# Kernel optimization log

Hardware: AMD Instinct MI355X
Metric: run time of the kernel (lower is better)

The kernel has to match this reference:

```python
import jax, jax.numpy as jnp
import numpy as np

# TT config: input_dimension=2048, output_multiplier=4, rank=16
# top_ranks    = [8,2,2,2,2,2,2,2,2]  (prod = 2048)
# bottom_ranks = [8,2,2,2,2,2,2,2,2]  (prod = 2048)
# core shapes (top, bottom, left, right): left/right are TT bond ranks.
CORE_SHAPES = [(8, 8, 1, 16)] + [(2, 2, 16, 16)] * 7 + [(2, 2, 16, 1)]


def setup_inputs() -> dict:
    key = jax.random.key(0)
    ks = jax.random.split(key, 10)
    inp = {"x": jax.random.normal(ks[0], (4, 2048, 2048), dtype=jnp.float32)}
    for i, s in enumerate(CORE_SHAPES):
        inp[f"p{i}"] = jax.random.normal(ks[i + 1], s, dtype=jnp.float32)
    return inp


def _tt_apply(x, ps):
    # x: [B, S, D] with D = prod(top_ranks) = 2048
    B, S, D = x.shape
    T = B * S
    # Normalize every core to (top, bottom, left_bond_in, right_bond_out).
    # Original einsum: '... abcdefghi, ajs, bkst, cltu, dmuv, envw, fowx, gpxy, hqzy, irz -> ... jklmnopqr'
    # Core 7 ('hqzy') has swapped bonds: its 4th dim (y) is the incoming bond
    # from core 6 and its 3rd dim (z) is the outgoing bond into core 8 ('irz').
    cores = list(ps[:7]) + [jnp.transpose(ps[7], (0, 1, 3, 2)), ps[8]]
    # core 0 is used as p0[:, :, 0, :] in the original; its left dim is 1 so
    # keeping the singleton left axis is identical math.
    y = x.reshape(T, 1, 1, D)  # [T, out_so_far=1, bond=1, remaining_top=D]
    J, M = 1, D
    for g in cores:
        tk, bk, lk, rk = g.shape
        y = y.reshape(T, J, lk, tk, M // tk)
        # contract incoming bond l and current top index a with the core
        y = jnp.einsum('tjlam,ablr->tjbrm', y, g)
        J *= bk
        M //= tk
        y = y.reshape(T, J, rk, M)
    # final: rk == 1, M == 1 -> [T, J] with J = prod(bottom_ranks) = 2048
    return y.reshape(B, S, J)


def reference(x, p0, p1, p2, p3, p4, p5, p6, p7, p8):
    return _tt_apply(x, (p0, p1, p2, p3, p4, p5, p6, p7, p8))
```

## Files before the change

kernel.cpp:

```cpp
#include <hip/hip_runtime.h>
#include <stdint.h>

typedef unsigned short u16;
typedef __bf16 bf16x8 __attribute__((ext_vector_type(8)));
typedef float f32x16 __attribute__((ext_vector_type(16)));
typedef u16 u16x8 __attribute__((ext_vector_type(8)));

__device__ __forceinline__ u16 f2bf(float f) {
  uint32_t u = __float_as_uint(f);
  u += 0x7fffu + ((u >> 16) & 1u);
  return (u16)(u >> 16);
}

__global__ __launch_bounds__(256) void build_lr_kernel(
    const float* __restrict__ p0, const float* __restrict__ p1,
    const float* __restrict__ p2, const float* __restrict__ p3,
    const float* __restrict__ p4, const float* __restrict__ p5,
    const float* __restrict__ p6, const float* __restrict__ p7,
    const float* __restrict__ p8, float* __restrict__ L4, float* __restrict__ R) {
  __shared__ float sA[16384];
  __shared__ float sB[4096];
  const int tid = threadIdx.x;
  if (blockIdx.x < 16) {
    for (int i = tid; i < 1024; i += 256) sA[i] = p0[i];
    __syncthreads();
    for (int i = tid; i < 4096; i += 256) {
      int r = i & 15, t = i >> 4;
      int Bb = t & 15, Aa = t >> 4;
      int a = Aa & 1, A = Aa >> 1, b = Bb & 1, B = Bb >> 1;
      const float* srow = sA + (A * 8 + B) * 16;
      const float* g = p1 + ((a * 2 + b) * 16) * 16 + r;
      float s = 0.f;
#pragma unroll
      for (int l = 0; l < 16; l++) s += srow[l] * g[l * 16];
      sB[i] = s;
    }
    __syncthreads();
    for (int i = tid; i < 16384; i += 256) {
      int r = i & 15, t = i >> 4;
      int Bb = t & 31, Aa = t >> 5;
      int a = Aa & 1, A = Aa >> 1, b = Bb & 1, B = Bb >> 1;
      const float* srow = sB + (A * 16 + B) * 16;
      const float* g = p2 + ((a * 2 + b) * 16) * 16 + r;
      float s = 0.f;
#pragma unroll
      for (int l = 0; l < 16; l++) s += srow[l] * g[l * 16];
      sA[i] = s;
    }
    __syncthreads();
    int gi = blockIdx.x * 256 + tid;
    int b3 = gi & 1, a3 = (gi >> 1) & 1;
    int B2 = (gi >> 2) & 31, A2 = gi >> 7;
    const float* srow = sA + (A2 * 32 + B2) * 16;
    const float* g3 = p3 + ((a3 * 2 + b3) * 16) * 16;
    float tmp[16];
#pragma unroll
    for (int r3 = 0; r3 < 16; r3++) {
      float s = 0.f;
#pragma unroll
      for (int r2 = 0; r2 < 16; r2++) s += srow[r2] * g3[r2 * 16 + r3];
      tmp[r3] = s;
    }
#pragma unroll
    for (int ab = 0; ab < 4; ab++) {
      int a4 = ab >> 1, b4 = ab & 1;
      const float* g4 = p4 + (ab * 16) * 16;
      int AL = A2 * 4 + a3 * 2 + a4;
      int BL = B2 * 4 + b3 * 2 + b4;
      float* drow = L4 + (AL * 128 + BL) * 16;
#pragma unroll
      for (int r4 = 0; r4 < 16; r4++) {
        float s = 0.f;
#pragma unroll
        for (int r3 = 0; r3 < 16; r3++) s += tmp[r3] * g4[r3 * 16 + r4];
        drow[r4] = s;
      }
    }
  } else {
    for (int i = tid; i < 64; i += 256) sA[i] = p8[i];
    __syncthreads();
    for (int i = tid; i < 256; i += 256) {
      int rl = i & 15, t = i >> 4;
      int Bt = t & 3, At = t >> 2;
      int a = At >> 1, Ap = At & 1, b = Bt >> 1, Bp = Bt & 1;
      const float* srow = sA + (Ap * 2 + Bp) * 16;
      const float* g = p7 + ((a * 2 + b) * 16) * 16 + rl;
      float s = 0.f;
#pragma unroll
      for (int rk = 0; rk < 16; rk++) s += srow[rk] * g[rk * 16];
      sB[i] = s;
    }
    __syncthreads();
    for (int i = tid; i < 1024; i += 256) {
      int rl = i & 15, t = i >> 4;
      int Bt = t & 7, At = t >> 3;
      int a = At >> 2, Ap = At & 3, b = Bt >> 2, Bp = Bt & 3;
      const float* srow = sB + (Ap * 4 + Bp) * 16;
      const float* g = p6 + (((a * 2 + b) * 16) + rl) * 16;
      float s = 0.f;
#pragma unroll
      for (int rk = 0; rk < 16; rk++) s += srow[rk] * g[rk];
      sA[i] = s;
    }
    __syncthreads();
    for (int i = tid; i < 4096; i += 256) {
      int rl = i & 15, t = i >> 4;
      int Bt = t & 15, At = t >> 4;
      int a = At >> 3, Ap = At & 7, b = Bt >> 3, Bp = Bt & 7;
      const float* srow = sA + (Ap * 8 + Bp) * 16;
      const float* g = p5 + (((a * 2 + b) * 16) + rl) * 16;
      float s = 0.f;
#pragma unroll
      for (int rk = 0; rk < 16; rk++) s += srow[rk] * g[rk];
      R[i] = s;
    }
  }
}

__global__ __launch_bounds__(256) void prep_kernel(const float* __restrict__ L4,
                                                   const float* __restrict__ R,
                                                   u16* __restrict__ Wt,
                                                   const float* __restrict__ x,
                                                   u16* __restrict__ xb) {
  if (blockIdx.x < 2048) {
    int t = blockIdx.x * 256 + threadIdx.x;
    int e = t * 8;
    int Af = e & 2047;
    int Bf = e >> 11;
    const float* lrow = L4 + ((Af >> 4) * 128 + (Bf >> 4)) * 16;
    float lv[16];
#pragma unroll
    for (int r = 0; r < 16; r++) lv[r] = lrow[r];
    const float* rbase = R + (Bf & 15) * 16;
    u16x8 o;
#pragma unroll
    for (int j = 0; j < 8; j++) {
      const float* rrow = rbase + ((Af + j) & 15) * 256;
      float s = 0.f;
#pragma unroll
      for (int r = 0; r < 16; r++) s += lv[r] * rrow[r];
      o[j] = f2bf(s);
    }
    *(u16x8*)(Wt + (size_t)Bf * 2048 + Af) = o;
  } else {
    size_t i = ((size_t)(blockIdx.x - 2048) * 256 + threadIdx.x) * 8;
    float4 u = *(const float4*)(x + i);
    float4 v = *(const float4*)(x + i + 4);
    u16x8 o;
    o[0] = f2bf(u.x); o[1] = f2bf(u.y); o[2] = f2bf(u.z); o[3] = f2bf(u.w);
    o[4] = f2bf(v.x); o[5] = f2bf(v.y); o[6] = f2bf(v.z); o[7] = f2bf(v.w);
    *(u16x8*)(xb + i) = o;
  }
}

#define SB0() __builtin_amdgcn_sched_barrier(0)
#define LGKM(n) asm volatile("s_waitcnt lgkmcnt(" #n ")" ::: "memory")
#define VMCW(n) asm volatile("s_waitcnt vmcnt(" #n ")" ::: "memory")
#define BAR() asm volatile("s_barrier" ::: "memory")

#define STAGE1(Sbase, dsto, gp, uoff)                                          \
  __builtin_amdgcn_global_load_lds(                                            \
      (const __attribute__((address_space(1))) void*)((gp) + (uoff) + pl),     \
      (__attribute__((address_space(3))) void*)((Sbase) + (dsto) + ldst), 16, 0, 0)

#define STAGE_A(h, dsto, gk)                                                   \
  STAGE1(As, (dsto), A, uA + ((h)*128) * 2048 + (gk));                         \
  STAGE1(As, (dsto) + 4096, A, uA + ((h)*128 + 64) * 2048 + (gk))

#define STAGE_B(h, dsto, gk)                                                   \
  STAGE1(Bs, (dsto), B, uB + ((h)*128) * 2048 + (gk));                         \
  STAGE1(Bs, (dsto) + 4096, B, uB + ((h)*128 + 64) * 2048 + (gk))

#define LOAD_AF_H(dst, ah, m, pav)                                             \
  _Pragma("unroll") for (int ks = 0; ks < 4; ks++)                             \
      dst[ks] = *(const bf16x8*)(As + (pav) + (ah)*8192 + rbA + (m)*2048 +     \
                                 (((ks * 2 + hl) ^ key) * 8))

#define LOAD_BV(dst, bh, pav)                                                  \
  _Pragma("unroll") for (int ks = 0; ks < 4; ks++)                             \
      dst[ks] = *(const bf16x8*)(Bs + (pav) + (bh)*8192 + rbB +                \
                                 (((ks * 2 + hl) ^ key) * 8))

#define MFMA4(afh, bvv, accv)                                                  \
  _Pragma("unroll") for (int ks = 0; ks < 4; ks++)                             \
      accv = __builtin_amdgcn_mfma_f32_32x32x16_bf16(afh[ks], bvv[ks], accv, 0, 0, 0)

#define MFMA8I(afarr, bvv, accp)                                               \
  _Pragma("unroll") for (int ks = 0; ks < 4; ks++) {                           \
    accp[0] = __builtin_amdgcn_mfma_f32_32x32x16_bf16(afarr[0][ks], bvv[ks], accp[0], 0, 0, 0); \
    accp[1] = __builtin_amdgcn_mfma_f32_32x32x16_bf16(afarr[1][ks], bvv[ks], accp[1], 0, 0, 0); \
  }

__global__ __launch_bounds__(512, 2) void gemm_kernel(const u16* __restrict__ A,
                                                      const u16* __restrict__ B,
                                                      float* __restrict__ C) {
  __shared__ alignas(128) u16 As[4 * 8192];
  __shared__ alignas(128) u16 Bs[4 * 8192];
  const int tid = threadIdx.x;
  const int lane = tid & 63;
  const int w = tid >> 6;
  const int wr = w >> 2;
  const int wc = w & 3;
  const int r32 = lane & 31;
  const int hl = lane >> 5;

  const int F = blockIdx.x + (blockIdx.y << 3);
  const int li = F >> 3;
  const int m0 = ((F & 7) * 4 + (li >> 3)) << 8;
  const int n0 = (li & 7) << 8;

  const int srow = lane >> 3;
  const int soct = (lane & 7) ^ srow;
  const int uA = m0 * 2048;
  const int uB = n0 * 2048;
  const int pl = (w * 8 + srow) * 2048 + soct * 8;
  const int ldst = w * 512;

  const int key = r32 & 7;
  const int rbA = (wr * 64 + r32) * 64;
  const int rbB = (wc * 32 + r32) * 64;

  f32x16 acc[2][2][2] = {};
  bf16x8 af[2][4], bv0[4], bv1[4];

  STAGE_A(0, 0, 0);      SB0();
  STAGE_B(1, 8192, 0);   SB0();
  STAGE_A(1, 8192, 0);   SB0();
  STAGE_B(0, 0, 0);      SB0();
  STAGE_A(0, 16384, 64); SB0();
  STAGE_B(1, 24576, 64); SB0();
  STAGE_A(1, 24576, 64); SB0();
  VMCW(6);
  BAR();
  LOAD_BV(bv0, 0, 0);
  SB0();

#pragma unroll 1
  for (int t = 0; t < 32; t++) {
    const int pav = (t & 1) << 14;
    const int pnv = 16384 - pav;
    const int k1 = (t < 31 ? t + 1 : 31) * 64;
    const int k2 = (t < 30 ? t + 2 : 31) * 64;
    STAGE_B(0, pnv, k1);
    SB0();
    LOAD_AF_H(af[0], 0, 0, pav); SB0();
    LOAD_AF_H(af[1], 0, 1, pav); SB0();
    LOAD_BV(bv1, 1, pav);
    LGKM(8); SB0();
    __builtin_amdgcn_s_setprio(1);
    MFMA4(af[0], bv0, acc[0][0][0]);
    LGKM(4); SB0();
    MFMA4(af[1], bv0, acc[0][0][1]);
    __builtin_amdgcn_s_setprio(0);
    BAR();
    STAGE_A(0, pav, k2);
    LGKM(0); SB0();
    __builtin_amdgcn_s_setprio(1);
    MFMA8I(af, bv1, acc[0][1]);
    __builtin_amdgcn_s_setprio(0);
    BAR();
    STAGE_B(1, pav + 8192, k2);
    SB0();
    LOAD_AF_H(af[0], 1, 0, pav); SB0();
    LOAD_AF_H(af[1], 1, 1, pav);
    LGKM(4); SB0();
    __builtin_amdgcn_s_setprio(1);
    MFMA4(af[0], bv1, acc[1][1][0]);
    LGKM(0); SB0();
    MFMA4(af[1], bv1, acc[1][1][1]);
    __builtin_amdgcn_s_setprio(0);
    BAR();
    STAGE_A(1, pav + 8192, k2);
    SB0();
    __builtin_amdgcn_s_setprio(1);
    MFMA8I(af, bv0, acc[1][0]);
    __builtin_amdgcn_s_setprio(0);
    VMCW(6);
    BAR();
    LOAD_BV(bv0, 0, pnv);
    SB0();
  }

  VMCW(0);

#pragma unroll
  for (int ah = 0; ah < 2; ah++)
#pragma unroll
    for (int bh = 0; bh < 2; bh++)
#pragma unroll
      for (int m = 0; m < 2; m++) {
        size_t cbase = (size_t)(m0 + ah * 128 + wr * 64 + m * 32 + 4 * hl) * 2048 +
                       (n0 + bh * 128 + wc * 32 + r32);
#pragma unroll
        for (int reg = 0; reg < 16; reg++) {
          int row = (reg & 3) + 8 * (reg >> 2);
          __builtin_nontemporal_store(acc[ah][bh][m][reg], C + cbase + (size_t)row * 2048);
        }
      }
}

extern "C" void kernel_launch(void* const* d_in, const int* in_sizes, int n_in,
                              void* d_out, int out_size, void* d_ws, size_t ws_size,
                              hipStream_t stream) {
  const float* x = (const float*)d_in[0];
  const float* p0 = (const float*)d_in[1];
  const float* p1 = (const float*)d_in[2];
  const float* p2 = (const float*)d_in[3];
  const float* p3 = (const float*)d_in[4];
  const float* p4 = (const float*)d_in[5];
  const float* p5 = (const float*)d_in[6];
  const float* p6 = (const float*)d_in[7];
  const float* p7 = (const float*)d_in[8];
  const float* p8 = (const float*)d_in[9];
  char* ws = (char*)d_ws;
  u16* xbf = (u16*)ws;
  u16* Wt = (u16*)(ws + 33554432);
  float* L4 = (float*)(ws + 41943040);
  float* R = (float*)(ws + 42991616);

  build_lr_kernel<<<17, 256, 0, stream>>>(p0, p1, p2, p3, p4, p5, p6, p7, p8, L4, R);
  prep_kernel<<<10240, 256, 0, stream>>>(L4, R, Wt, x, xbf);
  gemm_kernel<<<dim3(8, 32), 512, 0, stream>>>(xbf, Wt, (float*)d_out);
}
```

Measured before the change: 270.3 us.

## Recompute left TT chain per thread from shared cores across 64 blocks

Each thread of the left-factor build now computes its own L4 row by chaining cores 0-4 in registers, using all five cores staged once in shared memory. This drops the staged shared-memory intermediates and their barriers, and spreads the work over 64 blocks instead of 16. The right-factor branch likewise chains cores 8 to 5 per thread in registers. The cost is redundant recomputation of shared prefixes of the chain, but the aim is to cut the latency of the small serial setup kernel that sits before prep and the GEMM.

```diff
diff --git a/kernel.cpp b/kernel.cpp
--- a/kernel.cpp
+++ b/kernel.cpp
@@ -18,101 +18,86 @@
     const float* __restrict__ p4, const float* __restrict__ p5,
     const float* __restrict__ p6, const float* __restrict__ p7,
     const float* __restrict__ p8, float* __restrict__ L4, float* __restrict__ R) {
-  __shared__ float sA[16384];
-  __shared__ float sB[4096];
+  __shared__ float sC[5 * 1024];
   const int tid = threadIdx.x;
-  if (blockIdx.x < 16) {
-    for (int i = tid; i < 1024; i += 256) sA[i] = p0[i];
+  if (blockIdx.x < 64) {
+    for (int i = tid; i < 1024; i += 256) {
+      sC[i]        = p0[i];
+      sC[1024 + i] = p1[i];
+      sC[2048 + i] = p2[i];
+      sC[3072 + i] = p3[i];
+      sC[4096 + i] = p4[i];
+    }
     __syncthreads();
-    for (int i = tid; i < 4096; i += 256) {
-      int r = i & 15, t = i >> 4;
-      int Bb = t & 15, Aa = t >> 4;
-      int a = Aa & 1, A = Aa >> 1, b = Bb & 1, B = Bb >> 1;
-      const float* srow = sA + (A * 8 + B) * 16;
-      const float* g = p1 + ((a * 2 + b) * 16) * 16 + r;
+    const int idx = blockIdx.x * 256 + tid;
+    const int AL = idx >> 7, BL = idx & 127;
+    float t[16], u[16];
+    const float* c0 = sC + ((AL >> 4) * 8 + (BL >> 4)) * 16;
+#pragma unroll
+    for (int l = 0; l < 16; l++) t[l] = c0[l];
+#pragma unroll
+    for (int k = 0; k < 4; k++) {
+      const int ak = (AL >> (3 - k)) & 1;
+      const int bk = (BL >> (3 - k)) & 1;
+      const float* ck = sC + (k + 1) * 1024 + ((ak * 2 + bk) << 8);
+#pragma unroll
+      for (int r = 0; r < 16; r++) u[r] = 0.f;
+#pragma unroll
+      for (int l = 0; l < 16; l++) {
+        const float tv = t[l];
+#pragma unroll
+        for (int r = 0; r < 16; r++) u[r] += tv * ck[l * 16 + r];
+      }
+#pragma unroll
+      for (int r = 0; r < 16; r++) t[r] = u[r];
+    }
+    float4* dst = (float4*)(L4 + (size_t)idx * 16);
+#pragma unroll
+    for (int j = 0; j < 4; j++)
+      dst[j] = make_float4(t[4 * j], t[4 * j + 1], t[4 * j + 2], t[4 * j + 3]);
+  } else {
+    for (int i = tid; i < 1024; i += 256) {
+      sC[i]        = p5[i];
+      sC[1024 + i] = p6[i];
+      sC[2048 + i] = p7[i];
+    }
+    for (int i = tid; i < 64; i += 256) sC[3072 + i] = p8[i];
+    __syncthreads();
+    const int AR = tid >> 4, BR = tid & 15;
+    const int a5 = AR >> 3, a6 = (AR >> 2) & 1, a7 = (AR >> 1) & 1, a8 = AR & 1;
+    const int b5 = BR >> 3, b6 = (BR >> 2) & 1, b7 = (BR >> 1) & 1, b8 = BR & 1;
+    float t[16], u[16];
+    const float* c8 = sC + 3072 + (a8 * 2 + b8) * 16;
+#pragma unroll
+    for (int l = 0; l < 16; l++) t[l] = c8[l];
+    const float* c7 = sC + 2048 + ((a7 * 2 + b7) << 8);
+#pragma unroll
+    for (int r = 0; r < 16; r++) u[r] = 0.f;
+#pragma unroll
+    for (int z = 0; z < 16; z++) {
+      const float tv = t[z];
+#pragma unroll
+      for (int y = 0; y < 16; y++) u[y] += tv * c7[z * 16 + y];
+    }
+#pragma unroll
+    for (int r = 0; r < 16; r++) t[r] = u[r];
+    const float* c6 = sC + 1024 + ((a6 * 2 + b6) << 8);
+#pragma unroll
+    for (int rl = 0; rl < 16; rl++) {
       float s = 0.f;
 #pragma unroll
-      for (int l = 0; l < 16; l++) s += srow[l] * g[l * 16];
-      sB[i] = s;
-    }
-    __syncthreads();
-    for (int i = tid; i < 16384; i += 256) {
-      int r = i & 15, t = i >> 4;
-      int Bb = t & 31, Aa = t >> 5;
-      int a = Aa & 1, A = Aa >> 1, b = Bb & 1, B = Bb >> 1;
-      const float* srow = sB + (A * 16 + B) * 16;
-      const float* g = p2 + ((a * 2 + b) * 16) * 16 + r;
+      for (int rk = 0; rk < 16; rk++) s += t[rk] * c6[rl * 16 + rk];
+      u[rl] = s;
+    }
+#pragma unroll
+    for (int r = 0; r < 16; r++) t[r] = u[r];
+    const float* c5 = sC + ((a5 * 2 + b5) << 8);
+#pragma unroll
+    for (int rl = 0; rl < 16; rl++) {
       float s = 0.f;
 #pragma unroll
-      for (int l = 0; l < 16; l++) s += srow[l] * g[l * 16];
-      sA[i] = s;
-    }
-    __syncthreads();
-    int gi = blockIdx.x * 256 + tid;
-    int b3 = gi & 1, a3 = (gi >> 1) & 1;
-    int B2 = (gi >> 2) & 31, A2 = gi >> 7;
-    const float* srow = sA + (A2 * 32 + B2) * 16;
-    const float* g3 = p3 + ((a3 * 2 + b3) * 16) * 16;
-    float tmp[16];
-#pragma unroll
-    for (int r3 = 0; r3 < 16; r3++) {
-      float s = 0.f;
-#pragma unroll
-      for (int r2 = 0; r2 < 16; r2++) s += srow[r2] * g3[r2 * 16 + r3];
-      tmp[r3] = s;
-    }
-#pragma unroll
-    for (int ab = 0; ab < 4; ab++) {
-      int a4 = ab >> 1, b4 = ab & 1;
-      const float* g4 = p4 + (ab * 16) * 16;
-      int AL = A2 * 4 + a3 * 2 + a4;
-      int BL = B2 * 4 + b3 * 2 + b4;
-      float* drow = L4 + (AL * 128 + BL) * 16;
-#pragma unroll
-      for (int r4 = 0; r4 < 16; r4++) {
-        float s = 0.f;
-#pragma unroll
-        for (int r3 = 0; r3 < 16; r3++) s += tmp[r3] * g4[r3 * 16 + r4];
-        drow[r4] = s;
-      }
-    }
-  } else {
-    for (int i = tid; i < 64; i += 256) sA[i] = p8[i];
-    __syncthreads();
-    for (int i = tid; i < 256; i += 256) {
-      int rl = i & 15, t = i >> 4;
-      int Bt = t & 3, At = t >> 2;
-      int a = At >> 1, Ap = At & 1, b = Bt >> 1, Bp = Bt & 1;
-      const float* srow = sA + (Ap * 2 + Bp) * 16;
-      const float* g = p7 + ((a * 2 + b) * 16) * 16 + rl;
-      float s = 0.f;
-#pragma unroll
-      for (int rk = 0; rk < 16; rk++) s += srow[rk] * g[rk * 16];
-      sB[i] = s;
-    }
-    __syncthreads();
-    for (int i = tid; i < 1024; i += 256) {
-      int rl = i & 15, t = i >> 4;
-      int Bt = t & 7, At = t >> 3;
-      int a = At >> 2, Ap = At & 3, b = Bt >> 2, Bp = Bt & 3;
-      const float* srow = sB + (Ap * 4 + Bp) * 16;
-      const float* g = p6 + (((a * 2 + b) * 16) + rl) * 16;
-      float s = 0.f;
-#pragma unroll
-      for (int rk = 0; rk < 16; rk++) s += srow[rk] * g[rk];
-      sA[i] = s;
-    }
-    __syncthreads();
-    for (int i = tid; i < 4096; i += 256) {
-      int rl = i & 15, t = i >> 4;
-      int Bt = t & 15, At = t >> 4;
-      int a = At >> 3, Ap = At & 7, b = Bt >> 3, Bp = Bt & 7;
-      const float* srow = sA + (Ap * 8 + Bp) * 16;
-      const float* g = p5 + (((a * 2 + b) * 16) + rl) * 16;
-      float s = 0.f;
-#pragma unroll
-      for (int rk = 0; rk < 16; rk++) s += srow[rk] * g[rk];
-      R[i] = s;
+      for (int rk = 0; rk < 16; rk++) s += t[rk] * c5[rl * 16 + rk];
+      R[tid * 16 + rl] = s;
     }
   }
 }
@@ -318,7 +303,7 @@
   float* L4 = (float*)(ws + 41943040);
   float* R = (float*)(ws + 42991616);
 
-  build_lr_kernel<<<17, 256, 0, stream>>>(p0, p1, p2, p3, p4, p5, p6, p7, p8, L4, R);
+  build_lr_kernel<<<65, 256, 0, stream>>>(p0, p1, p2, p3, p4, p5, p6, p7, p8, L4, R);
   prep_kernel<<<10240, 256, 0, stream>>>(L4, R, Wt, x, xbf);
   gemm_kernel<<<dim3(8, 32), 512, 0, stream>>>(xbf, Wt, (float*)d_out);
 }
```

After: 224.7 us. 1.2x faster.
